# Optimization experiments

Measured on AMD Instinct MI355X. Metric: run time of the kernel, lower is better.

## Reference

```python
import jax, jax.numpy as jnp
import numpy as np

N = 100000      # nodes (PF candidates)
E = 1600000     # edges, avg degree 16
CONT = 6        # continuous features
H = 32          # hidden_dim
PDGS = [1, 2, 11, 13, 22, 130, 211]


def _p(k, shape):
    return jax.random.normal(k, shape, jnp.float32) * 0.1


def setup_inputs() -> dict:
    key = jax.random.key(0)
    ks = jax.random.split(key, 24)
    x_cont = jax.random.normal(ks[0], (N, CONT), jnp.float32)
    pdg = jnp.array(PDGS, jnp.int32)[jax.random.randint(ks[1], (N,), 0, 7)]
    sign = jax.random.randint(ks[2], (N,), 0, 2) * 2 - 1
    charge = jax.random.randint(ks[3], (N,), -1, 2)
    pv = jax.random.randint(ks[4], (N,), 0, 8)
    x_cat = jnp.stack([pdg * sign, charge, pv], axis=1).astype(jnp.int32)
    edge_index = jax.random.randint(ks[5], (2, E), 0, N, jnp.int32)
    batch = jnp.zeros((N,), jnp.int32)
    return {
        "x_cont": x_cont, "x_cat": x_cat, "edge_index": edge_index, "batch": batch,
        "W_cont": _p(ks[6], (CONT, H // 2)), "b_cont": jnp.zeros((H // 2,), jnp.float32),
        "T_chrg": _p(ks[7], (3, H // 4)), "T_pdg": _p(ks[8], (7, H // 4)), "T_pv": _p(ks[9], (8, H // 4)),
        "W_cat": _p(ks[10], (3 * H // 4, H // 2)), "b_cat": jnp.zeros((H // 2,), jnp.float32),
        "W_enc": _p(ks[11], (H, H)), "b_enc": jnp.zeros((H,), jnp.float32),
        "g_all": jnp.ones((H,), jnp.float32), "be_all": jnp.zeros((H,), jnp.float32),
        "W_msg": _p(ks[12], (2 * H, H)), "b_msg": jnp.zeros((H,), jnp.float32),
        "g_conv": jnp.ones((H,), jnp.float32), "be_conv": jnp.zeros((H,), jnp.float32),
        "W_out1": _p(ks[13], (H, H // 2)), "b_out1": jnp.zeros((H // 2,), jnp.float32),
        "W_out2": _p(ks[14], (H // 2, 1)), "b_out2": jnp.zeros((1,), jnp.float32),
    }


def _batchnorm(x, gamma, beta, eps=1e-5):
    # training-mode BatchNorm1d: biased batch stats over the node axis
    mu = jnp.mean(x, axis=0)
    var = jnp.mean(jnp.square(x - mu), axis=0)
    return (x - mu) * jax.lax.rsqrt(var + eps) * gamma + beta


def reference(x_cont, x_cat, edge_index, batch,
              W_cont, b_cont, T_chrg, T_pdg, T_pv, W_cat, b_cat,
              W_enc, b_enc, g_all, be_all, W_msg, b_msg, g_conv, be_conv,
              W_out1, b_out1, W_out2, b_out2):
    elu = jax.nn.elu
    emb_cont = elu(x_cont @ W_cont + b_cont)                      # [N, H/2]
    emb_chrg = T_chrg[x_cat[:, 1] + 1]                            # [N, H/4]
    emb_pv = T_pv[x_cat[:, 2]]                                    # [N, H/4]
    pdg_remap = jnp.abs(x_cat[:, 0])
    for i, pdgval in enumerate(PDGS):  # fixed small constant loop, as in original
        pdg_remap = jnp.where(pdg_remap == pdgval, jnp.int32(i), pdg_remap)
    emb_pdg = T_pdg[pdg_remap]                                    # [N, H/4]
    emb_cat = elu(jnp.concatenate([emb_chrg, emb_pdg, emb_pv], axis=1) @ W_cat + b_cat)
    emb = elu(jnp.concatenate([emb_cat, emb_cont], axis=1) @ W_enc + b_enc)
    emb = _batchnorm(emb, g_all, be_all)                          # [N, H]
    # EdgeConv: m_ij = nn([x_i, x_j - x_i]), aggregate by max over incoming edges
    src, dst = edge_index[0], edge_index[1]
    x_i = emb[dst]
    x_j = emb[src]
    msg = jnp.concatenate([x_i, x_j - x_i], axis=1) @ W_msg + b_msg   # [E, H]
    agg = jax.ops.segment_max(msg, dst, num_segments=N)
    agg = jnp.where(jnp.isfinite(agg), agg, 0.0)                  # nodes w/o in-edges -> 0
    emb = emb + _batchnorm(agg, g_conv, be_conv)
    out = elu(emb @ W_out1 + b_out1) @ W_out2 + b_out2            # [N, 1]
    return out.squeeze(-1)
```

## Files before the change

kernel.cpp:

```cpp
#include <hip/hip_runtime.h>
#include <hip/hip_bf16.h>

#define NN 100000
#define EE 1600000
#define NB_SCAN 391

#define NBUCK 782
#define CPAD  16
#define NPART 391
#define NE4   400000
#define CAP   4096
#define CAPSH 12
#define BCAP  2560

typedef __hip_bfloat16 bf16_t;
typedef int int4v __attribute__((ext_vector_type(4)));
typedef float f4 __attribute__((ext_vector_type(4)));

#define PARB  600000
#define EMB   604480
#define PBUF  3804480
#define QBUF  7004480
#define ABUF  10204480
#define SOFF  13404480
#define PART2 (SOFF + 256)
#define CURS  (PART2 + 4096)
#define ROWP2 (CURS + 12512)
#define OFLB  (ROWP2 + 200000)
#define PEB   (OFLB + 3200004)
#define SRCB  (PEB + 3203072)

#define O_WCONT 0
#define O_BCONT 96
#define O_TCHRG 112
#define O_TPDG  136
#define O_TPV   192
#define O_WCAT  256
#define O_BCAT  640
#define O_WENC  656
#define O_BENC  1680
#define O_GALL  1712
#define O_BEALL 1744
#define O_WMSG  1776
#define O_BMSG  3824
#define O_GCONV 3856
#define O_BECONV 3888
#define O_WOUT1 3920
#define O_BOUT1 4432
#define O_WOUT2 4448
#define O_BOUT2 4464
#define NPAR    4465

__device__ __forceinline__ float bf(unsigned short u) {
    return __uint_as_float(((unsigned)u) << 16);
}
__device__ __forceinline__ f4 elu4(f4 v) {
    f4 r;
    r.x = v.x > 0.0f ? v.x : expm1f(v.x);
    r.y = v.y > 0.0f ? v.y : expm1f(v.y);
    r.z = v.z > 0.0f ? v.z : expm1f(v.z);
    r.w = v.w > 0.0f ? v.w : expm1f(v.w);
    return r;
}
__device__ __forceinline__ f4 f4max(f4 a, f4 b) {
    f4 r;
    r.x = fmaxf(a.x, b.x); r.y = fmaxf(a.y, b.y);
    r.z = fmaxf(a.z, b.z); r.w = fmaxf(a.w, b.w);
    return r;
}

struct InitArgs {
    const void* p[19];
    const unsigned short* wdet;
    int*        flagw;
    float*      par;
    int*        curs;
    float*      stats;
    float*      part;
    int*        ofl;
    int*        tcur;
};

__global__ __launch_bounds__(256) void k_init(InitArgs a)
{
    const int offs[20] = {O_WCONT,O_BCONT,O_TCHRG,O_TPDG,O_TPV,O_WCAT,O_BCAT,O_WENC,
                          O_BENC,O_GALL,O_BEALL,O_WMSG,O_BMSG,O_GCONV,O_BECONV,
                          O_WOUT1,O_BOUT1,O_WOUT2,O_BOUT2,NPAR};
    __shared__ int sflag;
    int b = blockIdx.x, tid = threadIdx.x;
    int g = b * 256 + tid;
    if (g < NBUCK) a.curs[g * CPAD] = g << CAPSH;
    if (g < 4096) a.part[g] = 0.0f;
    if (g < 128) a.stats[g] = 0.0f;
    if (g == 0) { a.ofl[0] = 0; *a.tcur = NBUCK << CAPSH; }
    if (b == 0) {
        if (tid == 0) sflag = 0;
        __syncthreads();
        int bad = 0;
        for (int i = tid; i < 1024; i += 256) {
            unsigned e = (a.wdet[i] >> 7) & 0xFFu;
            if (e >= 137u) bad = 1;
        }
        if (bad) atomicOr(&sflag, 1);
        __syncthreads();
        int f32 = sflag;
        if (tid == 0) *a.flagw = f32;
        for (int i = tid; i < NPAR; i += 256) {
            int t = 0;
            while (offs[t + 1] <= i) t++;
            int l = i - offs[t];
            const void* s = a.p[t];
            a.par[i] = f32 ? ((const float*)s)[l] : bf(((const unsigned short*)s)[l]);
        }
    }
}

struct SMemPart { int cnt[NBUCK]; int start[NBUCK]; };
struct SMemEmb  { float wc[96], bc[16], tc[24], tp[56], tv[64],
                  wcat[384], bcat[16], we[1024], be[32], ls[64]; };
union SMemA { SMemPart p; SMemEmb e; };

__global__ __launch_bounds__(256, 1) void k_fA(
    const int* __restrict__ eidx, int* __restrict__ curs,
    int* __restrict__ pe, int* __restrict__ ofl, int2* __restrict__ ofl2,
    const void* __restrict__ xc, const int* __restrict__ x_cat,
    const float* __restrict__ par, const int* __restrict__ flag,
    float* __restrict__ emb, float* __restrict__ stats)
{
    __shared__ alignas(16) SMemA sm;
    int tid = threadIdx.x;
    int b = blockIdx.x;

    if (b < NPART) {
        for (int i = tid; i < NBUCK; i += 256) sm.p.cnt[i] = 0;
        __syncthreads();
        const int4v* src4 = (const int4v*)eidx;
        const int4v* dst4 = (const int4v*)(eidx + EE);
        int i0 = b << 10;
        int i1 = i0 + 1024; if (i1 > NE4) i1 = NE4;
        for (int i = i0 + tid; i < i1; i += 256) {
            int4v d = dst4[i];
            atomicAdd(&sm.p.cnt[d.x >> 7], 1);
            atomicAdd(&sm.p.cnt[d.y >> 7], 1);
            atomicAdd(&sm.p.cnt[d.z >> 7], 1);
            atomicAdd(&sm.p.cnt[d.w >> 7], 1);
        }
        __syncthreads();
        for (int i = tid; i < NBUCK; i += 256) {
            int c = sm.p.cnt[i];
            sm.p.start[i] = c ? atomicAdd(&curs[i * CPAD], c) : 0;
        }
        __syncthreads();
        for (int i = tid; i < NBUCK; i += 256) sm.p.cnt[i] = 0;
        __syncthreads();
        for (int i = i0 + tid; i < i1; i += 256) {
            int4v s = src4[i];
            int4v d = dst4[i];
            #define PLACE(SS, DD) { \
                int bk = (DD) >> 7; \
                int r = atomicAdd(&sm.p.cnt[bk], 1); \
                int slot = sm.p.start[bk] + r; \
                int packed = ((SS) << 7) | ((DD) & 127); \
                if (slot < ((bk + 1) << CAPSH)) pe[slot] = packed; \
                else { int oi = atomicAdd(ofl, 1); ofl2[oi] = make_int2(bk, packed); } }
            PLACE(s.x, d.x) PLACE(s.y, d.y) PLACE(s.z, d.z) PLACE(s.w, d.w)
            #undef PLACE
        }
        return;
    }

    {
        float* s;
        s=sm.e.wc;   for(int i=tid;i<96;  i+=256) s[i]=par[O_WCONT+i];
        s=sm.e.bc;   for(int i=tid;i<16;  i+=256) s[i]=par[O_BCONT+i];
        s=sm.e.tc;   for(int i=tid;i<24;  i+=256) s[i]=par[O_TCHRG+i];
        s=sm.e.tp;   for(int i=tid;i<56;  i+=256) s[i]=par[O_TPDG+i];
        s=sm.e.tv;   for(int i=tid;i<64;  i+=256) s[i]=par[O_TPV+i];
        s=sm.e.wcat; for(int i=tid;i<384; i+=256) s[i]=par[O_WCAT+i];
        s=sm.e.bcat; for(int i=tid;i<16;  i+=256) s[i]=par[O_BCAT+i];
        s=sm.e.we;   for(int i=tid;i<1024;i+=256) s[i]=par[O_WENC+i];
        s=sm.e.be;   for(int i=tid;i<32;  i+=256) s[i]=par[O_BENC+i];
        if (tid < 64) sm.e.ls[tid] = 0.0f;
    }
    __syncthreads();

    int n = (b - NPART) * 256 + tid;
    f4 esum[8], esq[8];
    #pragma unroll
    for (int g = 0; g < 8; g++) { esum[g] = (f4){0,0,0,0}; esq[g] = (f4){0,0,0,0}; }

    if (n < NN) {
        f4* sWc4 = (f4*)sm.e.wc;  f4* sbc4 = (f4*)sm.e.bc;
        f4* sTc4 = (f4*)sm.e.tc;  f4* sTp4 = (f4*)sm.e.tp;  f4* sTv4 = (f4*)sm.e.tv;
        f4* sWcat4 = (f4*)sm.e.wcat; f4* sbcat4 = (f4*)sm.e.bcat;
        f4* sWe4 = (f4*)sm.e.we;  f4* sbe4 = (f4*)sm.e.be;

        float x0,x1,x2,x3,x4,x5;
        if (*flag) {
            const float* xr = (const float*)xc + (size_t)n * 6;
            x0=xr[0]; x1=xr[1]; x2=xr[2]; x3=xr[3]; x4=xr[4]; x5=xr[5];
        } else {
            const unsigned* xr = (const unsigned*)xc + (size_t)n * 3;
            unsigned w0=xr[0], w1=xr[1], w2=xr[2];
            x0=__uint_as_float(w0<<16); x1=__uint_as_float(w0 & 0xFFFF0000u);
            x2=__uint_as_float(w1<<16); x3=__uint_as_float(w1 & 0xFFFF0000u);
            x4=__uint_as_float(w2<<16); x5=__uint_as_float(w2 & 0xFFFF0000u);
        }

        f4 ec[4];
        #pragma unroll
        for (int g = 0; g < 4; g++) {
            f4 acc = sbc4[g];
            acc += x0 * sWc4[0*4+g]; acc += x1 * sWc4[1*4+g]; acc += x2 * sWc4[2*4+g];
            acc += x3 * sWc4[3*4+g]; acc += x4 * sWc4[4*4+g]; acc += x5 * sWc4[5*4+g];
            ec[g] = elu4(acc);
        }

        int c0 = x_cat[n*3+0], c1 = x_cat[n*3+1], c2 = x_cat[n*3+2];
        int a0 = c0 < 0 ? -c0 : c0;
        int pi = (a0==1)?0:(a0==2)?1:(a0==11)?2:(a0==13)?3:(a0==22)?4:(a0==130)?5:6;
        int ci = c1 + 1;

        f4 t0a = sTc4[ci*2],  t0b = sTc4[ci*2+1];
        f4 t1a = sTp4[pi*2],  t1b = sTp4[pi*2+1];
        f4 t2a = sTv4[c2*2],  t2b = sTv4[c2*2+1];

        f4 ecat[4];
        #pragma unroll
        for (int g = 0; g < 4; g++) {
            f4 acc = sbcat4[g];
            #pragma unroll
            for (int k = 0; k < 4; k++) acc += t0a[k] * sWcat4[(k     )*4+g];
            #pragma unroll
            for (int k = 0; k < 4; k++) acc += t0b[k] * sWcat4[(4 + k )*4+g];
            #pragma unroll
            for (int k = 0; k < 4; k++) acc += t1a[k] * sWcat4[(8 + k )*4+g];
            #pragma unroll
            for (int k = 0; k < 4; k++) acc += t1b[k] * sWcat4[(12 + k)*4+g];
            #pragma unroll
            for (int k = 0; k < 4; k++) acc += t2a[k] * sWcat4[(16 + k)*4+g];
            #pragma unroll
            for (int k = 0; k < 4; k++) acc += t2b[k] * sWcat4[(20 + k)*4+g];
            ecat[g] = elu4(acc);
        }

        f4* o = (f4*)(emb + (size_t)n * 32);
        #pragma unroll
        for (int cg = 0; cg < 8; cg++) {
            f4 acc = sbe4[cg];
            #pragma unroll
            for (int kg = 0; kg < 4; kg++) {
                #pragma unroll
                for (int k = 0; k < 4; k++)
                    acc += ecat[kg][k] * sWe4[(kg*4+k)*8 + cg];
            }
            #pragma unroll
            for (int kg = 0; kg < 4; kg++) {
                #pragma unroll
                for (int k = 0; k < 4; k++)
                    acc += ec[kg][k] * sWe4[(16 + kg*4+k)*8 + cg];
            }
            f4 v = elu4(acc);
            o[cg] = v;
            esum[cg] = v;
            esq[cg]  = v * v;
        }
    }

    #pragma unroll
    for (int off = 1; off < 64; off <<= 1) {
        #pragma unroll
        for (int g = 0; g < 8; g++) {
            esum[g].x += __shfl_xor(esum[g].x, off);
            esum[g].y += __shfl_xor(esum[g].y, off);
            esum[g].z += __shfl_xor(esum[g].z, off);
            esum[g].w += __shfl_xor(esum[g].w, off);
            esq[g].x  += __shfl_xor(esq[g].x,  off);
            esq[g].y  += __shfl_xor(esq[g].y,  off);
            esq[g].z  += __shfl_xor(esq[g].z,  off);
            esq[g].w  += __shfl_xor(esq[g].w,  off);
        }
    }
    if ((tid & 63) == 0) {
        #pragma unroll
        for (int g = 0; g < 8; g++) {
            #pragma unroll
            for (int k = 0; k < 4; k++) {
                atomicAdd(&sm.e.ls[g*4+k],      esum[g][k]);
                atomicAdd(&sm.e.ls[32+g*4+k],   esq[g][k]);
            }
        }
    }
    __syncthreads();
    if (tid < 64) atomicAdd(&stats[tid], sm.e.ls[tid]);
}

struct SMemCsr { int stage[BCAP]; int cnt[128]; int sc[128]; int ex[128]; int tl; };
struct SMemPq  { float wp[1024], wq[1024], bp[32], bq[32], ssc[32], ssh[32]; };
union SMemB { SMemCsr c; SMemPq q; };

__global__ __launch_bounds__(256) void k_fB(
    const int* __restrict__ curs, const int* __restrict__ pe,
    const int* __restrict__ ofl, const int2* __restrict__ ofl2,
    int* __restrict__ tcur, int2* __restrict__ rowp2, int* __restrict__ srcl,
    const float* __restrict__ emb, const float* __restrict__ stats,
    const float* __restrict__ par, float* __restrict__ P, float* __restrict__ Q)
{
    __shared__ alignas(16) SMemB sm;
    int tid = threadIdx.x;
    int b = blockIdx.x;

    if (b < NBUCK) {
        int beg = b << CAPSH;
        int m_res = curs[b * CPAD] - beg;
        int stored = m_res < CAP ? m_res : CAP;
        int no = ofl[0];
        if (tid < 128) sm.c.cnt[tid] = 0;
        __syncthreads();
        for (int i = tid; i < stored; i += 256) {
            int p = pe[beg + i];
            if (i < BCAP) sm.c.stage[i] = p;
            atomicAdd(&sm.c.cnt[p & 127], 1);
        }
        for (int j = tid; j < no; j += 256) {
            int2 oe = ofl2[j];
            if (oe.x == b) atomicAdd(&sm.c.cnt[oe.y & 127], 1);
        }
        __syncthreads();
        if (tid < 128) sm.c.sc[tid] = sm.c.cnt[tid];
        __syncthreads();
        for (int off = 1; off < 128; off <<= 1) {
            int x = (tid >= off && tid < 128) ? sm.c.sc[tid - off] : 0;
            __syncthreads();
            if (tid < 128) sm.c.sc[tid] += x;
            __syncthreads();
        }
        int obeg = beg;
        if (m_res > CAP) {
            if (tid == 0) sm.c.tl = atomicAdd(tcur, m_res);
            __syncthreads();
            obeg = sm.c.tl;
        }
        if (tid < 128) {
            int e0 = sm.c.sc[tid] - sm.c.cnt[tid];
            int deg = sm.c.cnt[tid];
            sm.c.ex[tid] = e0;
            int node = b * 128 + tid;
            if (node < NN) rowp2[node] = make_int2(obeg + e0, obeg + e0 + deg);
            sm.c.cnt[tid] = 0;
        }
        __syncthreads();
        for (int i = tid; i < stored; i += 256) {
            int p = (i < BCAP) ? sm.c.stage[i] : pe[beg + i];
            int dl = p & 127;
            int r = atomicAdd(&sm.c.cnt[dl], 1);
            srcl[obeg + sm.c.ex[dl] + r] = p >> 7;
        }
        for (int j = tid; j < no; j += 256) {
            int2 oe = ofl2[j];
            if (oe.x == b) {
                int dl = oe.y & 127;
                int r = atomicAdd(&sm.c.cnt[dl], 1);
                srcl[obeg + sm.c.ex[dl] + r] = oe.y >> 7;
            }
        }
        return;
    }

    if (tid < 32) {
        float mu  = stats[tid] * (1.0f / NN);
        float var = stats[32 + tid] * (1.0f / NN) - mu * mu;
        float s   = par[O_GALL + tid] * rsqrtf(var + 1e-5f);
        sm.q.ssc[tid] = s;
        sm.q.ssh[tid] = par[O_BEALL + tid] - mu * s;
    }
    __syncthreads();
    for (int e = tid; e < 1024; e += 256) {
        int k = e >> 5;
        float w1 = par[O_WMSG + e];
        float w2 = par[O_WMSG + 1024 + e];
        sm.q.wp[e] = sm.q.ssc[k] * (w1 - w2);
        sm.q.wq[e] = sm.q.ssc[k] * w2;
    }
    if (tid < 32) {
        float aP = par[O_BMSG + tid], aQ = 0.0f;
        for (int k = 0; k < 32; k++) {
            float w1 = par[O_WMSG + k*32 + tid];
            float w2 = par[O_WMSG + (k+32)*32 + tid];
            aP += sm.q.ssh[k] * (w1 - w2);
            aQ += sm.q.ssh[k] * w2;
        }
        sm.q.bp[tid] = aP;
        sm.q.bq[tid] = aQ;
    }
    __syncthreads();

    int n = (b - NBUCK) * 256 + tid;
    if (n >= NN) return;

    f4* sWP4 = (f4*)sm.q.wp; f4* sWQ4 = (f4*)sm.q.wq;
    f4* sbP4 = (f4*)sm.q.bp; f4* sbQ4 = (f4*)sm.q.bq;
    const f4* er = (const f4*)(emb + (size_t)n * 32);
    f4 e[8];
    #pragma unroll
    for (int g = 0; g < 8; g++) e[g] = er[g];
    f4* pr = (f4*)(P + (size_t)n * 32);
    f4* qr = (f4*)(Q + (size_t)n * 32);
    #pragma unroll
    for (int cg = 0; cg < 8; cg++) {
        f4 aP = sbP4[cg];
        f4 aQ = sbQ4[cg];
        #pragma unroll
        for (int kg = 0; kg < 8; kg++) {
            #pragma unroll
            for (int k = 0; k < 4; k++) {
                float ek = e[kg][k];
                aP += ek * sWP4[(kg*4+k)*8 + cg];
                aQ += ek * sWQ4[(kg*4+k)*8 + cg];
            }
        }
        pr[cg] = aP;
        qr[cg] = aQ;
    }
}

__global__ __launch_bounds__(256) void k_gather(
    const int2* __restrict__ rowp2, const int* __restrict__ srcl,
    const float* __restrict__ Q, const float* __restrict__ P,
    float* __restrict__ agg, float* __restrict__ part)
{
    __shared__ float ls[64];
    int tid = threadIdx.x;
    if (tid < 64) ls[tid] = 0.0f;
    __syncthreads();

    int lane = tid & 63;
    int wave = tid >> 6;
    int n = blockIdx.x * 4 + wave;
    int slice = lane >> 3;
    int cg    = lane & 7;
    int2 be = rowp2[n];
    int beg = be.x, end = be.y;
    const f4* Q4 = (const f4*)Q;

    f4 pv = (f4){0.f, 0.f, 0.f, 0.f};
    if (lane < 8 && end > beg) pv = ((const f4*)P)[(size_t)n * 8 + lane];

    f4 m = {-INFINITY, -INFINITY, -INFINITY, -INFINITY};
    for (int e = beg + slice; e < end; e += 32) {
        int e1 = min(e + 8,  end - 1);
        int e2 = min(e + 16, end - 1);
        int e3 = min(e + 24, end - 1);
        int s0 = __builtin_nontemporal_load(&srcl[e]);
        int s1 = __builtin_nontemporal_load(&srcl[e1]);
        int s2 = __builtin_nontemporal_load(&srcl[e2]);
        int s3 = __builtin_nontemporal_load(&srcl[e3]);
        f4 q0 = Q4[(size_t)s0 * 8 + cg];
        f4 q1 = Q4[(size_t)s1 * 8 + cg];
        f4 q2 = Q4[(size_t)s2 * 8 + cg];
        f4 q3 = Q4[(size_t)s3 * 8 + cg];
        q0 = f4max(q0, q1);
        q2 = f4max(q2, q3);
        m = f4max(m, f4max(q0, q2));
    }
    #pragma unroll
    for (int off = 8; off < 64; off <<= 1) {
        m.x = fmaxf(m.x, __shfl_xor(m.x, off));
        m.y = fmaxf(m.y, __shfl_xor(m.y, off));
        m.z = fmaxf(m.z, __shfl_xor(m.z, off));
        m.w = fmaxf(m.w, __shfl_xor(m.w, off));
    }
    if (lane < 8) {
        f4 o;
        if (end > beg) o = m + pv;
        else           o = (f4){0.f, 0.f, 0.f, 0.f};
        ((f4*)agg)[(size_t)n * 8 + lane] = o;
        atomicAdd(&ls[cg*4+0], o.x);
        atomicAdd(&ls[cg*4+1], o.y);
        atomicAdd(&ls[cg*4+2], o.z);
        atomicAdd(&ls[cg*4+3], o.w);
        atomicAdd(&ls[32+cg*4+0], o.x*o.x);
        atomicAdd(&ls[32+cg*4+1], o.y*o.y);
        atomicAdd(&ls[32+cg*4+2], o.z*o.z);
        atomicAdd(&ls[32+cg*4+3], o.w*o.w);
    }
    __syncthreads();
    if (tid < 64) atomicAdd(&part[(blockIdx.x & 63) * 64 + tid], ls[tid]);
}

__global__ __launch_bounds__(256, 1) void k_out(
    const float* __restrict__ emb, const float* __restrict__ agg,
    const float* __restrict__ par, const float* __restrict__ stats,
    const float* __restrict__ part,
    const int* __restrict__ flag, void* __restrict__ out)
{
    __shared__ f4 sW14[128];
    __shared__ f4 sb14[4], sW24[4];
    __shared__ f4 sc14[8], sh14[8], sc24[8], sh24[8];
    __shared__ float spart[64];
    __shared__ float sb2s;
    int tid = threadIdx.x;
    {
        float* s = (float*)sW14;
        for (int i = tid; i < 512; i += 256) s[i] = par[O_WOUT1 + i];
    }
    if (tid < 16) {
        ((float*)sb14)[tid] = par[O_BOUT1 + tid];
        ((float*)sW24)[tid] = par[O_WOUT2 + tid];
    }
    if (tid < 64) {
        float acc2 = 0.0f;
        #pragma unroll 8
        for (int r = 0; r < 64; r++) acc2 += part[r * 64 + tid];
        spart[tid] = acc2;
    }
    if (tid == 0) sb2s = par[O_BOUT2];
    __syncthreads();
    if (tid < 32) {
        float mu  = stats[tid] * (1.0f / NN);
        float var = stats[32 + tid] * (1.0f / NN) - mu * mu;
        float s   = par[O_GALL + tid] * rsqrtf(var + 1e-5f);
        ((float*)sc14)[tid] = s;
        ((float*)sh14)[tid] = par[O_BEALL + tid] - mu * s;
        float mu2  = spart[tid] * (1.0f / NN);
        float var2 = spart[32 + tid] * (1.0f / NN) - mu2 * mu2;
        float s2   = par[O_GCONV + tid] * rsqrtf(var2 + 1e-5f);
        ((float*)sc24)[tid] = s2;
        ((float*)sh24)[tid] = par[O_BECONV + tid] - mu2 * s2;
    }
    __syncthreads();

    int n = blockIdx.x * 256 + tid;
    if (n >= NN) return;

    const f4* er = (const f4*)(emb + (size_t)n * 32);
    const f4* ar = (const f4*)(agg + (size_t)n * 32);
    f4 h[8];
    #pragma unroll
    for (int g = 0; g < 8; g++) {
        f4 ev = er[g];
        f4 av = ar[g];
        h[g] = ev * sc14[g] + sh14[g] + av * sc24[g] + sh24[g];
    }
    f4 o1[4];
    #pragma unroll
    for (int g = 0; g < 4; g++) {
        f4 acc = sb14[g];
        #pragma unroll
        for (int kg = 0; kg < 8; kg++) {
            #pragma unroll
            for (int k = 0; k < 4; k++)
                acc += h[kg][k] * sW14[(kg*4+k)*4 + g];
        }
        o1[g] = elu4(acc);
    }
    float acc = sb2s;
    #pragma unroll
    for (int g = 0; g < 4; g++) {
        f4 p = o1[g] * sW24[g];
        acc += p.x + p.y + p.z + p.w;
    }

    if (*flag) ((float*)out)[n] = acc;
    else       ((bf16_t*)out)[n] = __float2bfloat16(acc);
}


extern "C" void kernel_launch(void* const* d_in, const int* in_sizes, int n_in,
                              void* d_out, int out_size, void* d_ws, size_t ws_size,
                              hipStream_t stream)
{
    const void* x_cont = d_in[0];
    const int* x_cat = (const int*)d_in[1];
    const int* eidx  = (const int*)d_in[2];

    float* ws    = (float*)d_ws;
    float* par   = ws + PARB;
    float* emb   = ws + EMB;
    float* P     = ws + PBUF;
    float* Q     = ws + QBUF;
    float* agg   = ws + ABUF;
    float* stats = ws + SOFF;
    int*   flag  = (int*)(stats + 128);
    float* part  = ws + PART2;
    int*   curs  = (int*)(ws + CURS);
    int2*  rowp2 = (int2*)(ws + ROWP2);
    int*   ofl   = (int*)(ws + OFLB);
    int2*  ofl2  = (int2*)(ws + OFLB + 2);
    int*   pe    = (int*)(ws + PEB);
    int*   srcl  = (int*)(ws + SRCB);
    int*   tcur  = (int*)(stats + 130);

    InitArgs ia;
    for (int t = 0; t < 19; t++) ia.p[t] = d_in[4 + t];
    ia.wdet = (const unsigned short*)d_in[11];
    ia.flagw = flag; ia.par = par; ia.curs = curs; ia.stats = stats;
    ia.part = part; ia.ofl = ofl; ia.tcur = tcur;
    k_init<<<NB_SCAN, 256, 0, stream>>>(ia);

    k_fA<<<NPART + NB_SCAN, 256, 0, stream>>>(eidx, curs, pe, ofl, ofl2,
                                              x_cont, x_cat, par, flag, emb, stats);
    k_fB<<<NBUCK + NB_SCAN, 256, 0, stream>>>(curs, pe, ofl, ofl2, tcur, rowp2, srcl,
                                              emb, stats, par, P, Q);
    k_gather<<<NN / 4, 256, 0, stream>>>(rowp2, srcl, Q, P, agg, part);
    k_out<<<NB_SCAN, 256, 0, stream>>>(emb, agg, par, stats, part, flag, d_out);
}
```

Measured before the change: 286.0 us.

## Replace CSR build and gather with bucketed LDS atomicMax on order-preserving keys

```diff
diff --git a/kernel.cpp b/kernel.cpp
--- a/kernel.cpp
+++ b/kernel.cpp
@@ -11,10 +11,11 @@
 #define NE4   400000
 #define CAP   4096
 #define CAPSH 12
-#define BCAP  2560
+#define KINIT 0x007FFFFFu
 
 typedef __hip_bfloat16 bf16_t;
 typedef int int4v __attribute__((ext_vector_type(4)));
+typedef unsigned u4 __attribute__((ext_vector_type(4)));
 typedef float f4 __attribute__((ext_vector_type(4)));
 
 #define PARB  600000
@@ -25,10 +26,8 @@
 #define SOFF  13404480
 #define PART2 (SOFF + 256)
 #define CURS  (PART2 + 4096)
-#define ROWP2 (CURS + 12512)
-#define OFLB  (ROWP2 + 200000)
+#define OFLB  (CURS + 12512)
 #define PEB   (OFLB + 3200004)
-#define SRCB  (PEB + 3203072)
 
 #define O_WCONT 0
 #define O_BCONT 96
@@ -62,11 +61,12 @@
     r.w = v.w > 0.0f ? v.w : expm1f(v.w);
     return r;
 }
-__device__ __forceinline__ f4 f4max(f4 a, f4 b) {
-    f4 r;
-    r.x = fmaxf(a.x, b.x); r.y = fmaxf(a.y, b.y);
-    r.z = fmaxf(a.z, b.z); r.w = fmaxf(a.w, b.w);
-    return r;
+__device__ __forceinline__ unsigned fkey(float f) {
+    unsigned u = __float_as_uint(f);
+    return u ^ (((unsigned)((int)u >> 31)) | 0x80000000u);
+}
+__device__ __forceinline__ float fdec(unsigned k) {
+    return (k & 0x80000000u) ? __uint_as_float(k ^ 0x80000000u) : __uint_as_float(~k);
 }
 
 struct InitArgs {
@@ -78,7 +78,6 @@
     float*      stats;
     float*      part;
     int*        ofl;
-    int*        tcur;
 };
 
 __global__ __launch_bounds__(256) void k_init(InitArgs a)
@@ -92,7 +91,7 @@
     if (g < NBUCK) a.curs[g * CPAD] = g << CAPSH;
     if (g < 4096) a.part[g] = 0.0f;
     if (g < 128) a.stats[g] = 0.0f;
-    if (g == 0) { a.ofl[0] = 0; *a.tcur = NBUCK << CAPSH; }
+    if (g == 0) a.ofl[0] = 0;
     if (b == 0) {
         if (tid == 0) sflag = 0;
         __syncthreads();
@@ -185,9 +184,9 @@
     __syncthreads();
 
     int n = (b - NPART) * 256 + tid;
-    f4 esum[8], esq[8];
-    #pragma unroll
-    for (int g = 0; g < 8; g++) { esum[g] = (f4){0,0,0,0}; esq[g] = (f4){0,0,0,0}; }
+    float v[64];
+    #pragma unroll
+    for (int i = 0; i < 64; i++) v[i] = 0.0f;
 
     if (n < NN) {
         f4* sWc4 = (f4*)sm.e.wc;  f4* sbc4 = (f4*)sm.e.bc;
@@ -260,152 +259,84 @@
                 for (int k = 0; k < 4; k++)
                     acc += ec[kg][k] * sWe4[(16 + kg*4+k)*8 + cg];
             }
-            f4 v = elu4(acc);
-            o[cg] = v;
-            esum[cg] = v;
-            esq[cg]  = v * v;
-        }
-    }
-
-    #pragma unroll
-    for (int off = 1; off < 64; off <<= 1) {
-        #pragma unroll
-        for (int g = 0; g < 8; g++) {
-            esum[g].x += __shfl_xor(esum[g].x, off);
-            esum[g].y += __shfl_xor(esum[g].y, off);
-            esum[g].z += __shfl_xor(esum[g].z, off);
-            esum[g].w += __shfl_xor(esum[g].w, off);
-            esq[g].x  += __shfl_xor(esq[g].x,  off);
-            esq[g].y  += __shfl_xor(esq[g].y,  off);
-            esq[g].z  += __shfl_xor(esq[g].z,  off);
-            esq[g].w  += __shfl_xor(esq[g].w,  off);
-        }
-    }
-    if ((tid & 63) == 0) {
-        #pragma unroll
-        for (int g = 0; g < 8; g++) {
+            f4 val = elu4(acc);
+            o[cg] = val;
             #pragma unroll
             for (int k = 0; k < 4; k++) {
-                atomicAdd(&sm.e.ls[g*4+k],      esum[g][k]);
-                atomicAdd(&sm.e.ls[32+g*4+k],   esq[g][k]);
-            }
-        }
-    }
+                v[cg*4+k]      = val[k];
+                v[32+cg*4+k]   = val[k] * val[k];
+            }
+        }
+    }
+
+    int lane = tid & 63;
+    #pragma unroll
+    for (int st = 0; st < 6; st++) {
+        int off = 1 << st;
+        int keep = (lane >> st) & 1;
+        int L2 = 32 >> st;
+        #pragma unroll
+        for (int i = 0; i < 32; i++) {
+            if (i < L2) {
+                float lo = v[i], hi = v[L2 + i];
+                float sent = keep ? lo : hi;
+                float got = __shfl_xor(sent, off);
+                v[i] = (keep ? hi : lo) + got;
+            }
+        }
+    }
+    int idx = ((lane&1)<<5)|((lane&2)<<3)|((lane&4)<<1)|((lane&8)>>1)|((lane&16)>>3)|((lane&32)>>5);
+    atomicAdd(&sm.e.ls[idx], v[0]);
     __syncthreads();
     if (tid < 64) atomicAdd(&stats[tid], sm.e.ls[tid]);
 }
 
-struct SMemCsr { int stage[BCAP]; int cnt[128]; int sc[128]; int ex[128]; int tl; };
-struct SMemPq  { float wp[1024], wq[1024], bp[32], bq[32], ssc[32], ssh[32]; };
-union SMemB { SMemCsr c; SMemPq q; };
-
 __global__ __launch_bounds__(256) void k_fB(
-    const int* __restrict__ curs, const int* __restrict__ pe,
-    const int* __restrict__ ofl, const int2* __restrict__ ofl2,
-    int* __restrict__ tcur, int2* __restrict__ rowp2, int* __restrict__ srcl,
-    const float* __restrict__ emb, const float* __restrict__ stats,
-    const float* __restrict__ par, float* __restrict__ P, float* __restrict__ Q)
+    const float* __restrict__ par, const float* __restrict__ stats,
+    const float* __restrict__ emb, float* __restrict__ P, unsigned* __restrict__ Qk)
 {
-    __shared__ alignas(16) SMemB sm;
+    __shared__ float wp[1024], wq[1024], bp[32], bq[32], ssc[32], ssh[32];
     int tid = threadIdx.x;
     int b = blockIdx.x;
-
-    if (b < NBUCK) {
-        int beg = b << CAPSH;
-        int m_res = curs[b * CPAD] - beg;
-        int stored = m_res < CAP ? m_res : CAP;
-        int no = ofl[0];
-        if (tid < 128) sm.c.cnt[tid] = 0;
-        __syncthreads();
-        for (int i = tid; i < stored; i += 256) {
-            int p = pe[beg + i];
-            if (i < BCAP) sm.c.stage[i] = p;
-            atomicAdd(&sm.c.cnt[p & 127], 1);
-        }
-        for (int j = tid; j < no; j += 256) {
-            int2 oe = ofl2[j];
-            if (oe.x == b) atomicAdd(&sm.c.cnt[oe.y & 127], 1);
-        }
-        __syncthreads();
-        if (tid < 128) sm.c.sc[tid] = sm.c.cnt[tid];
-        __syncthreads();
-        for (int off = 1; off < 128; off <<= 1) {
-            int x = (tid >= off && tid < 128) ? sm.c.sc[tid - off] : 0;
-            __syncthreads();
-            if (tid < 128) sm.c.sc[tid] += x;
-            __syncthreads();
-        }
-        int obeg = beg;
-        if (m_res > CAP) {
-            if (tid == 0) sm.c.tl = atomicAdd(tcur, m_res);
-            __syncthreads();
-            obeg = sm.c.tl;
-        }
-        if (tid < 128) {
-            int e0 = sm.c.sc[tid] - sm.c.cnt[tid];
-            int deg = sm.c.cnt[tid];
-            sm.c.ex[tid] = e0;
-            int node = b * 128 + tid;
-            if (node < NN) rowp2[node] = make_int2(obeg + e0, obeg + e0 + deg);
-            sm.c.cnt[tid] = 0;
-        }
-        __syncthreads();
-        for (int i = tid; i < stored; i += 256) {
-            int p = (i < BCAP) ? sm.c.stage[i] : pe[beg + i];
-            int dl = p & 127;
-            int r = atomicAdd(&sm.c.cnt[dl], 1);
-            srcl[obeg + sm.c.ex[dl] + r] = p >> 7;
-        }
-        for (int j = tid; j < no; j += 256) {
-            int2 oe = ofl2[j];
-            if (oe.x == b) {
-                int dl = oe.y & 127;
-                int r = atomicAdd(&sm.c.cnt[dl], 1);
-                srcl[obeg + sm.c.ex[dl] + r] = oe.y >> 7;
-            }
-        }
-        return;
-    }
-
     if (tid < 32) {
         float mu  = stats[tid] * (1.0f / NN);
         float var = stats[32 + tid] * (1.0f / NN) - mu * mu;
         float s   = par[O_GALL + tid] * rsqrtf(var + 1e-5f);
-        sm.q.ssc[tid] = s;
-        sm.q.ssh[tid] = par[O_BEALL + tid] - mu * s;
+        ssc[tid] = s;
+        ssh[tid] = par[O_BEALL + tid] - mu * s;
     }
     __syncthreads();
     for (int e = tid; e < 1024; e += 256) {
         int k = e >> 5;
         float w1 = par[O_WMSG + e];
         float w2 = par[O_WMSG + 1024 + e];
-        sm.q.wp[e] = sm.q.ssc[k] * (w1 - w2);
-        sm.q.wq[e] = sm.q.ssc[k] * w2;
+        wp[e] = ssc[k] * (w1 - w2);
+        wq[e] = ssc[k] * w2;
     }
     if (tid < 32) {
         float aP = par[O_BMSG + tid], aQ = 0.0f;
         for (int k = 0; k < 32; k++) {
             float w1 = par[O_WMSG + k*32 + tid];
             float w2 = par[O_WMSG + (k+32)*32 + tid];
-            aP += sm.q.ssh[k] * (w1 - w2);
-            aQ += sm.q.ssh[k] * w2;
-        }
-        sm.q.bp[tid] = aP;
-        sm.q.bq[tid] = aQ;
-    }
-    __syncthreads();
-
-    int n = (b - NBUCK) * 256 + tid;
+            aP += ssh[k] * (w1 - w2);
+            aQ += ssh[k] * w2;
+        }
+        bp[tid] = aP;
+        bq[tid] = aQ;
+    }
+    __syncthreads();
+
+    int n = b * 256 + tid;
     if (n >= NN) return;
 
-    f4* sWP4 = (f4*)sm.q.wp; f4* sWQ4 = (f4*)sm.q.wq;
-    f4* sbP4 = (f4*)sm.q.bp; f4* sbQ4 = (f4*)sm.q.bq;
+    f4* sWP4 = (f4*)wp; f4* sWQ4 = (f4*)wq;
+    f4* sbP4 = (f4*)bp; f4* sbQ4 = (f4*)bq;
     const f4* er = (const f4*)(emb + (size_t)n * 32);
     f4 e[8];
     #pragma unroll
     for (int g = 0; g < 8; g++) e[g] = er[g];
     f4* pr = (f4*)(P + (size_t)n * 32);
-    f4* qr = (f4*)(Q + (size_t)n * 32);
+    u4* qr = (u4*)(Qk + (size_t)n * 32);
     #pragma unroll
     for (int cg = 0; cg < 8; cg++) {
         f4 aP = sbP4[cg];
@@ -420,72 +351,93 @@
             }
         }
         pr[cg] = aP;
-        qr[cg] = aQ;
-    }
-}
-
-__global__ __launch_bounds__(256) void k_gather(
-    const int2* __restrict__ rowp2, const int* __restrict__ srcl,
-    const float* __restrict__ Q, const float* __restrict__ P,
+        u4 qk;
+        qk.x = fkey(aQ.x); qk.y = fkey(aQ.y);
+        qk.z = fkey(aQ.z); qk.w = fkey(aQ.w);
+        qr[cg] = qk;
+    }
+}
+
+__global__ __launch_bounds__(256) void k_gmax(
+    const int* __restrict__ curs, const int* __restrict__ pe,
+    const int* __restrict__ ofl, const int2* __restrict__ ofl2,
+    const unsigned* __restrict__ Qk, const float* __restrict__ P,
     float* __restrict__ agg, float* __restrict__ part)
 {
+    __shared__ unsigned sK[4096];
     __shared__ float ls[64];
     int tid = threadIdx.x;
+    int b = blockIdx.x;
+
+    #pragma unroll
+    for (int i = 0; i < 16; i++) sK[tid + i * 256] = KINIT;
     if (tid < 64) ls[tid] = 0.0f;
     __syncthreads();
 
-    int lane = tid & 63;
-    int wave = tid >> 6;
-    int n = blockIdx.x * 4 + wave;
-    int slice = lane >> 3;
-    int cg    = lane & 7;
-    int2 be = rowp2[n];
-    int beg = be.x, end = be.y;
-    const f4* Q4 = (const f4*)Q;
-
-    f4 pv = (f4){0.f, 0.f, 0.f, 0.f};
-    if (lane < 8 && end > beg) pv = ((const f4*)P)[(size_t)n * 8 + lane];
-
-    f4 m = {-INFINITY, -INFINITY, -INFINITY, -INFINITY};
-    for (int e = beg + slice; e < end; e += 32) {
-        int e1 = min(e + 8,  end - 1);
-        int e2 = min(e + 16, end - 1);
-        int e3 = min(e + 24, end - 1);
-        int s0 = __builtin_nontemporal_load(&srcl[e]);
-        int s1 = __builtin_nontemporal_load(&srcl[e1]);
-        int s2 = __builtin_nontemporal_load(&srcl[e2]);
-        int s3 = __builtin_nontemporal_load(&srcl[e3]);
-        f4 q0 = Q4[(size_t)s0 * 8 + cg];
-        f4 q1 = Q4[(size_t)s1 * 8 + cg];
-        f4 q2 = Q4[(size_t)s2 * 8 + cg];
-        f4 q3 = Q4[(size_t)s3 * 8 + cg];
-        q0 = f4max(q0, q1);
-        q2 = f4max(q2, q3);
-        m = f4max(m, f4max(q0, q2));
-    }
-    #pragma unroll
-    for (int off = 8; off < 64; off <<= 1) {
-        m.x = fmaxf(m.x, __shfl_xor(m.x, off));
-        m.y = fmaxf(m.y, __shfl_xor(m.y, off));
-        m.z = fmaxf(m.z, __shfl_xor(m.z, off));
-        m.w = fmaxf(m.w, __shfl_xor(m.w, off));
-    }
-    if (lane < 8) {
-        f4 o;
-        if (end > beg) o = m + pv;
-        else           o = (f4){0.f, 0.f, 0.f, 0.f};
-        ((f4*)agg)[(size_t)n * 8 + lane] = o;
-        atomicAdd(&ls[cg*4+0], o.x);
-        atomicAdd(&ls[cg*4+1], o.y);
-        atomicAdd(&ls[cg*4+2], o.z);
-        atomicAdd(&ls[cg*4+3], o.w);
-        atomicAdd(&ls[32+cg*4+0], o.x*o.x);
-        atomicAdd(&ls[32+cg*4+1], o.y*o.y);
-        atomicAdd(&ls[32+cg*4+2], o.z*o.z);
-        atomicAdd(&ls[32+cg*4+3], o.w*o.w);
-    }
-    __syncthreads();
-    if (tid < 64) atomicAdd(&part[(blockIdx.x & 63) * 64 + tid], ls[tid]);
+    int beg = b << CAPSH;
+    int m = curs[b * CPAD] - beg;
+    int stored = m < CAP ? m : CAP;
+    const u4* Qk4 = (const u4*)Qk;
+
+    for (int i = tid; i < stored; i += 256) {
+        int p = pe[beg + i];
+        int src = p >> 7, dl = p & 127;
+        #pragma unroll
+        for (int g = 0; g < 8; g++) {
+            u4 q = Qk4[(size_t)src * 8 + g];
+            atomicMax(&sK[(g*4+0)*128 + dl], q.x);
+            atomicMax(&sK[(g*4+1)*128 + dl], q.y);
+            atomicMax(&sK[(g*4+2)*128 + dl], q.z);
+            atomicMax(&sK[(g*4+3)*128 + dl], q.w);
+        }
+    }
+    int no = ofl[0];
+    for (int j = tid; j < no; j += 256) {
+        int2 oe = ofl2[j];
+        if (oe.x == b) {
+            int p = oe.y;
+            int src = p >> 7, dl = p & 127;
+            #pragma unroll
+            for (int g = 0; g < 8; g++) {
+                u4 q = Qk4[(size_t)src * 8 + g];
+                atomicMax(&sK[(g*4+0)*128 + dl], q.x);
+                atomicMax(&sK[(g*4+1)*128 + dl], q.y);
+                atomicMax(&sK[(g*4+2)*128 + dl], q.z);
+                atomicMax(&sK[(g*4+3)*128 + dl], q.w);
+            }
+        }
+    }
+    __syncthreads();
+
+    int nl = tid >> 1;
+    int ch0 = (tid & 1) * 16;
+    int node = b * 128 + nl;
+    if (node < NN) {
+        bool has = (sK[nl] != KINIT);
+        const f4* P4 = (const f4*)P;
+        f4* A4 = (f4*)agg;
+        #pragma unroll
+        for (int g = 0; g < 4; g++) {
+            int ch = ch0 + g * 4;
+            f4 o;
+            if (has) {
+                o.x = fdec(sK[(ch+0)*128 + nl]);
+                o.y = fdec(sK[(ch+1)*128 + nl]);
+                o.z = fdec(sK[(ch+2)*128 + nl]);
+                o.w = fdec(sK[(ch+3)*128 + nl]);
+                o += P4[(size_t)node * 8 + (ch >> 2)];
+            } else {
+                o = (f4){0.f, 0.f, 0.f, 0.f};
+            }
+            A4[(size_t)node * 8 + (ch >> 2)] = o;
+            atomicAdd(&ls[ch+0], o.x); atomicAdd(&ls[32+ch+0], o.x*o.x);
+            atomicAdd(&ls[ch+1], o.y); atomicAdd(&ls[32+ch+1], o.y*o.y);
+            atomicAdd(&ls[ch+2], o.z); atomicAdd(&ls[32+ch+2], o.z*o.z);
+            atomicAdd(&ls[ch+3], o.w); atomicAdd(&ls[32+ch+3], o.w*o.w);
+        }
+    }
+    __syncthreads();
+    if (tid < 64) atomicAdd(&part[(b & 63) * 64 + tid], ls[tid]);
 }
 
 __global__ __launch_bounds__(256, 1) void k_out(
@@ -574,34 +526,30 @@
     const int* x_cat = (const int*)d_in[1];
     const int* eidx  = (const int*)d_in[2];
 
-    float* ws    = (float*)d_ws;
-    float* par   = ws + PARB;
-    float* emb   = ws + EMB;
-    float* P     = ws + PBUF;
-    float* Q     = ws + QBUF;
-    float* agg   = ws + ABUF;
-    float* stats = ws + SOFF;
-    int*   flag  = (int*)(stats + 128);
-    float* part  = ws + PART2;
-    int*   curs  = (int*)(ws + CURS);
-    int2*  rowp2 = (int2*)(ws + ROWP2);
-    int*   ofl   = (int*)(ws + OFLB);
-    int2*  ofl2  = (int2*)(ws + OFLB + 2);
-    int*   pe    = (int*)(ws + PEB);
-    int*   srcl  = (int*)(ws + SRCB);
-    int*   tcur  = (int*)(stats + 130);
+    float*    ws    = (float*)d_ws;
+    float*    par   = ws + PARB;
+    float*    emb   = ws + EMB;
+    float*    P     = ws + PBUF;
+    unsigned* Qk    = (unsigned*)(ws + QBUF);
+    float*    agg   = ws + ABUF;
+    float*    stats = ws + SOFF;
+    int*      flag  = (int*)(stats + 128);
+    float*    part  = ws + PART2;
+    int*      curs  = (int*)(ws + CURS);
+    int*      ofl   = (int*)(ws + OFLB);
+    int2*     ofl2  = (int2*)(ws + OFLB + 2);
+    int*      pe    = (int*)(ws + PEB);
 
     InitArgs ia;
     for (int t = 0; t < 19; t++) ia.p[t] = d_in[4 + t];
     ia.wdet = (const unsigned short*)d_in[11];
     ia.flagw = flag; ia.par = par; ia.curs = curs; ia.stats = stats;
-    ia.part = part; ia.ofl = ofl; ia.tcur = tcur;
+    ia.part = part; ia.ofl = ofl;
     k_init<<<NB_SCAN, 256, 0, stream>>>(ia);
 
     k_fA<<<NPART + NB_SCAN, 256, 0, stream>>>(eidx, curs, pe, ofl, ofl2,
                                               x_cont, x_cat, par, flag, emb, stats);
-    k_fB<<<NBUCK + NB_SCAN, 256, 0, stream>>>(curs, pe, ofl, ofl2, tcur, rowp2, srcl,
-                                              emb, stats, par, P, Q);
-    k_gather<<<NN / 4, 256, 0, stream>>>(rowp2, srcl, Q, P, agg, part);
+    k_fB<<<NB_SCAN, 256, 0, stream>>>(par, stats, emb, P, Qk);
+    k_gmax<<<NBUCK, 256, 0, stream>>>(curs, pe, ofl, ofl2, Qk, P, agg, part);
     k_out<<<NB_SCAN, 256, 0, stream>>>(emb, agg, par, stats, part, flag, d_out);
 }
```

Result: no change. 288.2 us (+0.8%).

## Stage bucketed edges in LDS for coalesced writes, transpose-reduce BN stats

Applied to the files above, without the earlier changes.

```diff
diff --git a/kernel.cpp b/kernel.cpp
--- a/kernel.cpp
+++ b/kernel.cpp
@@ -115,7 +115,14 @@
     }
 }
 
-struct SMemPart { int cnt[NBUCK]; int start[NBUCK]; };
+struct SMemPart {
+    int cnt[NBUCK];
+    int lstart[NBUCK];
+    int gstart[NBUCK];
+    int tsum[256];
+    unsigned short bkof[4096];
+    int staged[4096];
+};
 struct SMemEmb  { float wc[96], bc[16], tc[24], tp[56], tv[64],
                   wcat[384], bcat[16], we[1024], be[32], ls[64]; };
 union SMemA { SMemPart p; SMemEmb e; };
@@ -138,6 +145,7 @@
         const int4v* dst4 = (const int4v*)(eidx + EE);
         int i0 = b << 10;
         int i1 = i0 + 1024; if (i1 > NE4) i1 = NE4;
+        int nE = (i1 - i0) * 4;
         for (int i = i0 + tid; i < i1; i += 256) {
             int4v d = dst4[i];
             atomicAdd(&sm.p.cnt[d.x >> 7], 1);
@@ -146,25 +154,66 @@
             atomicAdd(&sm.p.cnt[d.w >> 7], 1);
         }
         __syncthreads();
+        int base = tid * 4;
+        int c0 = (base     < NBUCK) ? sm.p.cnt[base    ] : 0;
+        int c1 = (base + 1 < NBUCK) ? sm.p.cnt[base + 1] : 0;
+        int c2 = (base + 2 < NBUCK) ? sm.p.cnt[base + 2] : 0;
+        int c3 = (base + 3 < NBUCK) ? sm.p.cnt[base + 3] : 0;
+        int s = c0 + c1 + c2 + c3;
+        sm.p.tsum[tid] = s;
+        __syncthreads();
+        for (int off = 1; off < 256; off <<= 1) {
+            int x = (tid >= off) ? sm.p.tsum[tid - off] : 0;
+            __syncthreads();
+            sm.p.tsum[tid] += x;
+            __syncthreads();
+        }
+        int run = sm.p.tsum[tid] - s;
+        if (base < NBUCK) {
+            sm.p.lstart[base] = run;
+            if (c0) sm.p.gstart[base] = atomicAdd(&curs[base * CPAD], c0);
+            run += c0;
+        }
+        if (base + 1 < NBUCK) {
+            sm.p.lstart[base + 1] = run;
+            if (c1) sm.p.gstart[base + 1] = atomicAdd(&curs[(base + 1) * CPAD], c1);
+            run += c1;
+        }
+        if (base + 2 < NBUCK) {
+            sm.p.lstart[base + 2] = run;
+            if (c2) sm.p.gstart[base + 2] = atomicAdd(&curs[(base + 2) * CPAD], c2);
+            run += c2;
+        }
+        if (base + 3 < NBUCK) {
+            sm.p.lstart[base + 3] = run;
+            if (c3) sm.p.gstart[base + 3] = atomicAdd(&curs[(base + 3) * CPAD], c3);
+            run += c3;
+        }
+        __syncthreads();
         for (int i = tid; i < NBUCK; i += 256) {
-            int c = sm.p.cnt[i];
-            sm.p.start[i] = c ? atomicAdd(&curs[i * CPAD], c) : 0;
+            int st = sm.p.lstart[i], c = sm.p.cnt[i];
+            for (int j = 0; j < c; j++) sm.p.bkof[st + j] = (unsigned short)i;
         }
         __syncthreads();
         for (int i = tid; i < NBUCK; i += 256) sm.p.cnt[i] = 0;
         __syncthreads();
         for (int i = i0 + tid; i < i1; i += 256) {
-            int4v s = src4[i];
-            int4v d = dst4[i];
+            int4v s4 = src4[i];
+            int4v d4 = dst4[i];
             #define PLACE(SS, DD) { \
                 int bk = (DD) >> 7; \
                 int r = atomicAdd(&sm.p.cnt[bk], 1); \
-                int slot = sm.p.start[bk] + r; \
-                int packed = ((SS) << 7) | ((DD) & 127); \
-                if (slot < ((bk + 1) << CAPSH)) pe[slot] = packed; \
-                else { int oi = atomicAdd(ofl, 1); ofl2[oi] = make_int2(bk, packed); } }
-            PLACE(s.x, d.x) PLACE(s.y, d.y) PLACE(s.z, d.z) PLACE(s.w, d.w)
+                sm.p.staged[sm.p.lstart[bk] + r] = ((SS) << 7) | ((DD) & 127); }
+            PLACE(s4.x, d4.x) PLACE(s4.y, d4.y) PLACE(s4.z, d4.z) PLACE(s4.w, d4.w)
             #undef PLACE
+        }
+        __syncthreads();
+        for (int j = tid; j < nE; j += 256) {
+            int bk = sm.p.bkof[j];
+            int slot = sm.p.gstart[bk] + (j - sm.p.lstart[bk]);
+            int packed = sm.p.staged[j];
+            if (slot < ((bk + 1) << CAPSH)) pe[slot] = packed;
+            else { int oi = atomicAdd(ofl, 1); ofl2[oi] = make_int2(bk, packed); }
         }
         return;
     }
@@ -185,9 +234,9 @@
     __syncthreads();
 
     int n = (b - NPART) * 256 + tid;
-    f4 esum[8], esq[8];
-    #pragma unroll
-    for (int g = 0; g < 8; g++) { esum[g] = (f4){0,0,0,0}; esq[g] = (f4){0,0,0,0}; }
+    float v[64];
+    #pragma unroll
+    for (int i = 0; i < 64; i++) v[i] = 0.0f;
 
     if (n < NN) {
         f4* sWc4 = (f4*)sm.e.wc;  f4* sbc4 = (f4*)sm.e.bc;
@@ -260,37 +309,34 @@
                 for (int k = 0; k < 4; k++)
                     acc += ec[kg][k] * sWe4[(16 + kg*4+k)*8 + cg];
             }
-            f4 v = elu4(acc);
-            o[cg] = v;
-            esum[cg] = v;
-            esq[cg]  = v * v;
-        }
-    }
-
-    #pragma unroll
-    for (int off = 1; off < 64; off <<= 1) {
+            f4 val = elu4(acc);
+            o[cg] = val;
+            #pragma unroll
+            for (int k = 0; k < 4; k++) {
+                v[cg*4+k]      = val[k];
+                v[32+cg*4+k]   = val[k] * val[k];
+            }
+        }
+    }
+
+    int lane = tid & 63;
+    #pragma unroll
+    for (int st = 0; st < 6; st++) {
+        int off = 1 << st;
+        int keep = (lane >> st) & 1;
+        int L2 = 32 >> st;
         #pragma unroll
-        for (int g = 0; g < 8; g++) {
-            esum[g].x += __shfl_xor(esum[g].x, off);
-            esum[g].y += __shfl_xor(esum[g].y, off);
-            esum[g].z += __shfl_xor(esum[g].z, off);
-            esum[g].w += __shfl_xor(esum[g].w, off);
-            esq[g].x  += __shfl_xor(esq[g].x,  off);
-            esq[g].y  += __shfl_xor(esq[g].y,  off);
-            esq[g].z  += __shfl_xor(esq[g].z,  off);
-            esq[g].w  += __shfl_xor(esq[g].w,  off);
-        }
-    }
-    if ((tid & 63) == 0) {
-        #pragma unroll
-        for (int g = 0; g < 8; g++) {
-            #pragma unroll
-            for (int k = 0; k < 4; k++) {
-                atomicAdd(&sm.e.ls[g*4+k],      esum[g][k]);
-                atomicAdd(&sm.e.ls[32+g*4+k],   esq[g][k]);
+        for (int i = 0; i < 32; i++) {
+            if (i < L2) {
+                float lo = v[i], hi = v[L2 + i];
+                float sent = keep ? lo : hi;
+                float got = __shfl_xor(sent, off);
+                v[i] = (keep ? hi : lo) + got;
             }
         }
     }
+    int idx = ((lane&1)<<5)|((lane&2)<<3)|((lane&4)<<1)|((lane&8)>>1)|((lane&16)>>3)|((lane&32)>>5);
+    atomicAdd(&sm.e.ls[idx], v[0]);
     __syncthreads();
     if (tid < 64) atomicAdd(&stats[tid], sm.e.ls[tid]);
 }
@@ -582,6 +628,7 @@
     float* agg   = ws + ABUF;
     float* stats = ws + SOFF;
     int*   flag  = (int*)(stats + 128);
+    int*   tcur  = (int*)(stats + 130);
     float* part  = ws + PART2;
     int*   curs  = (int*)(ws + CURS);
     int2*  rowp2 = (int2*)(ws + ROWP2);
@@ -589,14 +636,13 @@
     int2*  ofl2  = (int2*)(ws + OFLB + 2);
     int*   pe    = (int*)(ws + PEB);
     int*   srcl  = (int*)(ws + SRCB);
-    int*   tcur  = (int*)(stats + 130);
 
     InitArgs ia;
     for (int t = 0; t < 19; t++) ia.p[t] = d_in[4 + t];
     ia.wdet = (const unsigned short*)d_in[11];
     ia.flagw = flag; ia.par = par; ia.curs = curs; ia.stats = stats;
     ia.part = part; ia.ofl = ofl; ia.tcur = tcur;
-    k_init<<<NB_SCAN, 256, 0, stream>>>(ia);
+    k_init<<<16, 256, 0, stream>>>(ia);
 
     k_fA<<<NPART + NB_SCAN, 256, 0, stream>>>(eidx, curs, pe, ofl, ofl2,
                                               x_cont, x_cat, par, flag, emb, stats);
```

After: 265.6 us. 1.08x faster.
